# Optimization experiments

Hardware: AMD Instinct MI355X
Metric: run time of the kernel (lower is better)

The kernel has to match this reference:

```python
import jax, jax.numpy as jnp
import numpy as np

TEMPERATURE = 0.07
EPS = 1e-8  # torch CosineSimilarity norm clamp

N, D, NUM_CLASSES = 4096, 768, 128


def setup_inputs() -> dict:
    key = jax.random.key(0)
    k1, k2, k3 = jax.random.split(key, 3)
    img_emb = jax.random.normal(k1, (N, D), dtype=jnp.float32)
    text_emb = jax.random.normal(k2, (N, D), dtype=jnp.float32)
    labels = jax.random.randint(k3, (N,), 0, NUM_CLASSES, dtype=jnp.int64)
    return {"img_emb": img_emb, "text_emb": text_emb, "labels": labels}


def reference(img_emb, text_emb, labels):
    # cosine similarity via normalize + matmul (avoids O(N^2 D) broadcast)
    img_n = img_emb / jnp.maximum(jnp.linalg.norm(img_emb, axis=-1, keepdims=True), EPS)
    txt_n = text_emb / jnp.maximum(jnp.linalg.norm(text_emb, axis=-1, keepdims=True), EPS)
    logits = jnp.einsum('id,jd->ij', img_n, txt_n) / TEMPERATURE  # [N, N]

    pos_mask = (labels[:, None] == labels[None, :]).astype(logits.dtype)  # [N, N]

    img2text = -(pos_mask * jax.nn.log_softmax(logits, axis=1)).sum(1).mean()
    text2img = -(pos_mask * jax.nn.log_softmax(logits, axis=0)).sum(0).mean()
    return (img2text + text2img) / 2
```

## Files before the change

### kernel.cpp

```cpp
#include <hip/hip_runtime.h>
#include <hip/hip_bf16.h>

#define N_ 4096
#define D_ 768
#define NCLS 128
#define BM 128
#define BN 128
#define BK 64
#define NSTEP 12

typedef __bf16 bf16x8 __attribute__((ext_vector_type(8)));
typedef float f32x4 __attribute__((ext_vector_type(4)));
typedef short s16x8 __attribute__((ext_vector_type(8)));

__global__ __launch_bounds__(192) void normalize_kernel(
    const float* __restrict__ img, const float* __restrict__ txt,
    __hip_bfloat16* __restrict__ img_nb, __hip_bfloat16* __restrict__ txt_nb) {
  int b = blockIdx.x;
  const float* s;
  __hip_bfloat16* d;
  if (b < N_) {
    s = img + (size_t)b * D_;
    d = img_nb + (size_t)b * D_;
  } else {
    s = txt + (size_t)(b - N_) * D_;
    d = txt_nb + (size_t)(b - N_) * D_;
  }
  int tid = threadIdx.x;
  float4 v = ((const float4*)s)[tid];
  float ss = v.x * v.x + v.y * v.y + v.z * v.z + v.w * v.w;
#pragma unroll
  for (int m = 32; m; m >>= 1) ss += __shfl_xor(ss, m);
  __shared__ float wsum[3];
  int lane = tid & 63, w = tid >> 6;
  if (lane == 0) wsum[w] = ss;
  __syncthreads();
  float inv = 1.0f / fmaxf(sqrtf(wsum[0] + wsum[1] + wsum[2]), 1e-8f);
  ushort4 o;
  o.x = __bfloat16_as_ushort(__float2bfloat16(v.x * inv));
  o.y = __bfloat16_as_ushort(__float2bfloat16(v.y * inv));
  o.z = __bfloat16_as_ushort(__float2bfloat16(v.z * inv));
  o.w = __bfloat16_as_ushort(__float2bfloat16(v.w * inv));
  ((ushort4*)d)[tid] = o;
}

__global__ __launch_bounds__(256) void gemm_epi_kernel(
    const unsigned short* __restrict__ A, const unsigned short* __restrict__ B,
    const int* __restrict__ labels, float* __restrict__ row_part,
    float* __restrict__ col_part, float* __restrict__ S_part) {
  __shared__ __align__(16) unsigned short As[2][8192];
  __shared__ __align__(16) unsigned short Bs[2][8192];
  __shared__ int labR[BM], labC[BN];
  __shared__ float rbuf[2][BM], cbuf[2][BN];
  __shared__ float sbuf[4];

  const int bx = blockIdx.x, by = blockIdx.y;
  const int tid = threadIdx.x;
  const int lane = tid & 63, wave = tid >> 6;
  const int wr = wave >> 1, wc = wave & 1;
  const int g = lane >> 4, fr = lane & 15;
  const int rowBase = by * BM, colBase = bx * BN;

  if (tid < BM) labR[tid] = labels[rowBase + tid];
  else labC[tid - BM] = labels[colBase + tid - BM];

  const int gq = tid & 7, rbase = tid >> 3;
  const unsigned short* pa = A + (size_t)(rowBase + rbase) * D_ + gq * 8;
  const unsigned short* pb = B + (size_t)(colBase + rbase) * D_ + gq * 8;
  const int wpos = (rbase * 8 + (gq ^ (rbase & 7))) * 8;

  f32x4 acc[4][4] = {};

  s16x8 ra[4], rb[4];
#pragma unroll
  for (int j = 0; j < 4; ++j) {
    ra[j] = *(const s16x8*)(pa + (size_t)(32 * j) * D_);
    rb[j] = *(const s16x8*)(pb + (size_t)(32 * j) * D_);
  }
#pragma unroll
  for (int j = 0; j < 4; ++j) {
    *(s16x8*)&As[0][wpos + j * 2048] = ra[j];
    *(s16x8*)&Bs[0][wpos + j * 2048] = rb[j];
  }
#pragma unroll
  for (int j = 0; j < 4; ++j) {
    ra[j] = *(const s16x8*)(pa + (size_t)(32 * j) * D_ + BK);
    rb[j] = *(const s16x8*)(pb + (size_t)(32 * j) * D_ + BK);
  }
  __syncthreads();

  for (int u = 0; u < NSTEP; ++u) {
    if (u + 1 < NSTEP) {
      unsigned short* aw = As[(u + 1) & 1];
      unsigned short* bw = Bs[(u + 1) & 1];
#pragma unroll
      for (int j = 0; j < 4; ++j) {
        *(s16x8*)&aw[wpos + j * 2048] = ra[j];
        *(s16x8*)&bw[wpos + j * 2048] = rb[j];
      }
    }
    const unsigned short* as_ = As[u & 1];
    const unsigned short* bs_ = Bs[u & 1];
#pragma unroll
    for (int ks = 0; ks < 2; ++ks) {
      const int sw = (ks * 4 + g) ^ (fr & 7);
      bf16x8 af[4], bf[4];
#pragma unroll
      for (int m = 0; m < 4; ++m)
        af[m] = *(const bf16x8*)&as_[((wr * 64 + m * 16 + fr) * 8 + sw) * 8];
#pragma unroll
      for (int n = 0; n < 4; ++n)
        bf[n] = *(const bf16x8*)&bs_[((wc * 64 + n * 16 + fr) * 8 + sw) * 8];
#pragma unroll
      for (int m = 0; m < 4; ++m)
#pragma unroll
        for (int n = 0; n < 4; ++n)
          acc[m][n] = __builtin_amdgcn_mfma_f32_16x16x32_bf16(af[m], bf[n], acc[m][n], 0, 0, 0);
    }
    if (u + 2 < NSTEP) {
      const int k0 = (u + 2) * BK;
#pragma unroll
      for (int j = 0; j < 4; ++j) {
        ra[j] = *(const s16x8*)(pa + (size_t)(32 * j) * D_ + k0);
        rb[j] = *(const s16x8*)(pb + (size_t)(32 * j) * D_ + k0);
      }
    }
    __syncthreads();
  }

  const float scale = 14.285714285714286f;
  float sPart = 0.f;
  float colAcc[4] = {0.f, 0.f, 0.f, 0.f};
#pragma unroll
  for (int m = 0; m < 4; ++m) {
    float ra2[4] = {0.f, 0.f, 0.f, 0.f};
#pragma unroll
    for (int n = 0; n < 4; ++n) {
      int col = wc * 64 + n * 16 + fr;
      int lc = labC[col];
#pragma unroll
      for (int r = 0; r < 4; ++r) {
        float v = acc[m][n][r] * scale;
        float e = __expf(v);
        ra2[r] += e;
        colAcc[n] += e;
        int row = wr * 64 + m * 16 + g * 4 + r;
        if (labR[row] == lc) sPart += v;
      }
    }
#pragma unroll
    for (int r = 0; r < 4; ++r) {
      float x = ra2[r];
      x += __shfl_xor(x, 1);
      x += __shfl_xor(x, 2);
      x += __shfl_xor(x, 4);
      x += __shfl_xor(x, 8);
      if (fr == 0) rbuf[wc][wr * 64 + m * 16 + g * 4 + r] = x;
    }
  }
#pragma unroll
  for (int n = 0; n < 4; ++n) {
    float x = colAcc[n];
    x += __shfl_xor(x, 16);
    x += __shfl_xor(x, 32);
    if (g == 0) cbuf[wr][wc * 64 + n * 16 + fr] = x;
  }
  float s = sPart;
#pragma unroll
  for (int m = 32; m; m >>= 1) s += __shfl_xor(s, m);
  if (lane == 0) sbuf[wave] = s;
  __syncthreads();
  if (tid < BM)
    row_part[(size_t)bx * N_ + rowBase + tid] = rbuf[0][tid] + rbuf[1][tid];
  else
    col_part[(size_t)by * N_ + colBase + (tid - BM)] = cbuf[0][tid - BM] + cbuf[1][tid - BM];
  if (tid == 0) S_part[by * 32 + bx] = sbuf[0] + sbuf[1] + sbuf[2] + sbuf[3];
}

__global__ __launch_bounds__(256) void reduce_kernel(
    const float* __restrict__ row_part, const float* __restrict__ col_part,
    const float* __restrict__ S_part, const int* __restrict__ labels,
    double* __restrict__ partials) {
  __shared__ int hist[NCLS];
  int tid = threadIdx.x;
  if (tid < NCLS) hist[tid] = 0;
  __syncthreads();
  for (int j = tid; j < N_; j += 256) atomicAdd(&hist[labels[j]], 1);
  __syncthreads();

  int i = blockIdx.x * 256 + tid;
  float rs = 0.f, cs = 0.f;
#pragma unroll
  for (int b = 0; b < 32; ++b) {
    rs += row_part[(size_t)b * N_ + i];
    cs += col_part[(size_t)b * N_ + i];
  }
  int cnt = hist[labels[i]];
  double term = (double)cnt * ((double)logf(rs) + (double)logf(cs));
  double sterm = (i < 1024) ? (double)S_part[i] : 0.0;
#pragma unroll
  for (int m = 32; m; m >>= 1) {
    term += __shfl_xor(term, m);
    sterm += __shfl_xor(sterm, m);
  }
  __shared__ double tbuf[4], sb[4];
  int lane = tid & 63, w = tid >> 6;
  if (lane == 0) { tbuf[w] = term; sb[w] = sterm; }
  __syncthreads();
  if (tid == 0) {
    partials[blockIdx.x] = tbuf[0] + tbuf[1] + tbuf[2] + tbuf[3];
    partials[16 + blockIdx.x] = sb[0] + sb[1] + sb[2] + sb[3];
  }
}

__global__ void final_kernel(const double* __restrict__ partials, float* __restrict__ out) {
  double t = 0.0, s = 0.0;
#pragma unroll
  for (int i = 0; i < 16; ++i) {
    t += partials[i];
    s += partials[16 + i];
  }
  out[0] = (float)((t - 2.0 * s) / (2.0 * (double)N_));
}

extern "C" void kernel_launch(void* const* d_in, const int* in_sizes, int n_in,
                              void* d_out, int out_size, void* d_ws, size_t ws_size,
                              hipStream_t stream) {
  const float* img = (const float*)d_in[0];
  const float* txt = (const float*)d_in[1];
  const int* labels = (const int*)d_in[2];
  float* out = (float*)d_out;
  char* ws = (char*)d_ws;

  __hip_bfloat16* img_nb = (__hip_bfloat16*)(ws);
  __hip_bfloat16* txt_nb = (__hip_bfloat16*)(ws + 6291456);
  float* row_part = (float*)(ws + 12582912);
  float* col_part = (float*)(ws + 13107200);
  float* S_part = (float*)(ws + 13631488);
  double* partials = (double*)(ws + 13635584);

  normalize_kernel<<<2 * N_, 192, 0, stream>>>(img, txt, img_nb, txt_nb);
  gemm_epi_kernel<<<dim3(32, 32), 256, 0, stream>>>(
      (const unsigned short*)img_nb, (const unsigned short*)txt_nb, labels,
      row_part, col_part, S_part);
  reduce_kernel<<<16, 256, 0, stream>>>(row_part, col_part, S_part, labels, partials);
  final_kernel<<<1, 1, 0, stream>>>(partials, out);
}
```

Baseline: 56.08 us.

## Use wave-per-row normalize, reorder GEMM LDS reads, fold final reduce into atomics

The normalize kernel now gives each 64-lane wave a whole row, which removes the shared-memory cross-wave reduction and its barrier. The GEMM loop issues the first k-slice LDS reads before the next-stage shared-memory stores, so MFMA work can overlap with those writes. The final single-thread kernel is replaced by a last-block-done pattern using double atomics plus a memset, removing one launch. The trade-off is an added memset launch and atomic ordering that depends on a threadfence.

Result: slower. 59.32 us (+5.8%).

```diff
diff --git a/kernel.cpp b/kernel.cpp
--- a/kernel.cpp
+++ b/kernel.cpp
@@ -13,35 +13,45 @@
 typedef float f32x4 __attribute__((ext_vector_type(4)));
 typedef short s16x8 __attribute__((ext_vector_type(8)));
 
-__global__ __launch_bounds__(192) void normalize_kernel(
+__global__ __launch_bounds__(256) void normalize_kernel(
     const float* __restrict__ img, const float* __restrict__ txt,
     __hip_bfloat16* __restrict__ img_nb, __hip_bfloat16* __restrict__ txt_nb) {
-  int b = blockIdx.x;
+  int idx = blockIdx.x * 4 + (threadIdx.x >> 6);
+  int lane = threadIdx.x & 63;
   const float* s;
   __hip_bfloat16* d;
-  if (b < N_) {
-    s = img + (size_t)b * D_;
-    d = img_nb + (size_t)b * D_;
+  if (idx < N_) {
+    s = img + (size_t)idx * D_;
+    d = img_nb + (size_t)idx * D_;
   } else {
-    s = txt + (size_t)(b - N_) * D_;
-    d = txt_nb + (size_t)(b - N_) * D_;
-  }
-  int tid = threadIdx.x;
-  float4 v = ((const float4*)s)[tid];
-  float ss = v.x * v.x + v.y * v.y + v.z * v.z + v.w * v.w;
+    s = txt + (size_t)(idx - N_) * D_;
+    d = txt_nb + (size_t)(idx - N_) * D_;
+  }
+  float4 v0 = ((const float4*)s)[lane];
+  float4 v1 = ((const float4*)s)[lane + 64];
+  float4 v2 = ((const float4*)s)[lane + 128];
+  float ss = v0.x * v0.x + v0.y * v0.y + v0.z * v0.z + v0.w * v0.w +
+             v1.x * v1.x + v1.y * v1.y + v1.z * v1.z + v1.w * v1.w +
+             v2.x * v2.x + v2.y * v2.y + v2.z * v2.z + v2.w * v2.w;
 #pragma unroll
   for (int m = 32; m; m >>= 1) ss += __shfl_xor(ss, m);
-  __shared__ float wsum[3];
-  int lane = tid & 63, w = tid >> 6;
-  if (lane == 0) wsum[w] = ss;
-  __syncthreads();
-  float inv = 1.0f / fmaxf(sqrtf(wsum[0] + wsum[1] + wsum[2]), 1e-8f);
-  ushort4 o;
-  o.x = __bfloat16_as_ushort(__float2bfloat16(v.x * inv));
-  o.y = __bfloat16_as_ushort(__float2bfloat16(v.y * inv));
-  o.z = __bfloat16_as_ushort(__float2bfloat16(v.z * inv));
-  o.w = __bfloat16_as_ushort(__float2bfloat16(v.w * inv));
-  ((ushort4*)d)[tid] = o;
+  float inv = 1.0f / fmaxf(sqrtf(ss), 1e-8f);
+  ushort4 o0, o1, o2;
+  o0.x = __bfloat16_as_ushort(__float2bfloat16(v0.x * inv));
+  o0.y = __bfloat16_as_ushort(__float2bfloat16(v0.y * inv));
+  o0.z = __bfloat16_as_ushort(__float2bfloat16(v0.z * inv));
+  o0.w = __bfloat16_as_ushort(__float2bfloat16(v0.w * inv));
+  o1.x = __bfloat16_as_ushort(__float2bfloat16(v1.x * inv));
+  o1.y = __bfloat16_as_ushort(__float2bfloat16(v1.y * inv));
+  o1.z = __bfloat16_as_ushort(__float2bfloat16(v1.z * inv));
+  o1.w = __bfloat16_as_ushort(__float2bfloat16(v1.w * inv));
+  o2.x = __bfloat16_as_ushort(__float2bfloat16(v2.x * inv));
+  o2.y = __bfloat16_as_ushort(__float2bfloat16(v2.y * inv));
+  o2.z = __bfloat16_as_ushort(__float2bfloat16(v2.z * inv));
+  o2.w = __bfloat16_as_ushort(__float2bfloat16(v2.w * inv));
+  ((ushort4*)d)[lane] = o0;
+  ((ushort4*)d)[lane + 64] = o1;
+  ((ushort4*)d)[lane + 128] = o2;
 }
 
 __global__ __launch_bounds__(256) void gemm_epi_kernel(
@@ -90,6 +100,18 @@
   __syncthreads();
 
   for (int u = 0; u < NSTEP; ++u) {
+    const unsigned short* as_ = As[u & 1];
+    const unsigned short* bs_ = Bs[u & 1];
+    bf16x8 af[4], bf[4];
+    {
+      const int sw = g ^ (fr & 7);
+#pragma unroll
+      for (int m = 0; m < 4; ++m)
+        af[m] = *(const bf16x8*)&as_[((wr * 64 + m * 16 + fr) * 8 + sw) * 8];
+#pragma unroll
+      for (int n = 0; n < 4; ++n)
+        bf[n] = *(const bf16x8*)&bs_[((wc * 64 + n * 16 + fr) * 8 + sw) * 8];
+    }
     if (u + 1 < NSTEP) {
       unsigned short* aw = As[(u + 1) & 1];
       unsigned short* bw = Bs[(u + 1) & 1];
@@ -99,24 +121,25 @@
         *(s16x8*)&bw[wpos + j * 2048] = rb[j];
       }
     }
-    const unsigned short* as_ = As[u & 1];
-    const unsigned short* bs_ = Bs[u & 1];
-#pragma unroll
-    for (int ks = 0; ks < 2; ++ks) {
-      const int sw = (ks * 4 + g) ^ (fr & 7);
-      bf16x8 af[4], bf[4];
+#pragma unroll
+    for (int m = 0; m < 4; ++m)
+#pragma unroll
+      for (int n = 0; n < 4; ++n)
+        acc[m][n] = __builtin_amdgcn_mfma_f32_16x16x32_bf16(af[m], bf[n], acc[m][n], 0, 0, 0);
+    {
+      const int sw = (4 + g) ^ (fr & 7);
 #pragma unroll
       for (int m = 0; m < 4; ++m)
         af[m] = *(const bf16x8*)&as_[((wr * 64 + m * 16 + fr) * 8 + sw) * 8];
 #pragma unroll
       for (int n = 0; n < 4; ++n)
         bf[n] = *(const bf16x8*)&bs_[((wc * 64 + n * 16 + fr) * 8 + sw) * 8];
-#pragma unroll
-      for (int m = 0; m < 4; ++m)
-#pragma unroll
-        for (int n = 0; n < 4; ++n)
-          acc[m][n] = __builtin_amdgcn_mfma_f32_16x16x32_bf16(af[m], bf[n], acc[m][n], 0, 0, 0);
-    }
+    }
+#pragma unroll
+    for (int m = 0; m < 4; ++m)
+#pragma unroll
+      for (int n = 0; n < 4; ++n)
+        acc[m][n] = __builtin_amdgcn_mfma_f32_16x16x32_bf16(af[m], bf[n], acc[m][n], 0, 0, 0);
     if (u + 2 < NSTEP) {
       const int k0 = (u + 2) * BK;
 #pragma unroll
@@ -180,7 +203,7 @@
 __global__ __launch_bounds__(256) void reduce_kernel(
     const float* __restrict__ row_part, const float* __restrict__ col_part,
     const float* __restrict__ S_part, const int* __restrict__ labels,
-    double* __restrict__ partials) {
+    double* __restrict__ accs, unsigned* __restrict__ cnt, float* __restrict__ out) {
   __shared__ int hist[NCLS];
   int tid = threadIdx.x;
   if (tid < NCLS) hist[tid] = 0;
@@ -195,8 +218,8 @@
     rs += row_part[(size_t)b * N_ + i];
     cs += col_part[(size_t)b * N_ + i];
   }
-  int cnt = hist[labels[i]];
-  double term = (double)cnt * ((double)logf(rs) + (double)logf(cs));
+  int c = hist[labels[i]];
+  double term = (double)c * ((double)logf(rs) + (double)logf(cs));
   double sterm = (i < 1024) ? (double)S_part[i] : 0.0;
 #pragma unroll
   for (int m = 32; m; m >>= 1) {
@@ -208,19 +231,16 @@
   if (lane == 0) { tbuf[w] = term; sb[w] = sterm; }
   __syncthreads();
   if (tid == 0) {
-    partials[blockIdx.x] = tbuf[0] + tbuf[1] + tbuf[2] + tbuf[3];
-    partials[16 + blockIdx.x] = sb[0] + sb[1] + sb[2] + sb[3];
-  }
-}
-
-__global__ void final_kernel(const double* __restrict__ partials, float* __restrict__ out) {
-  double t = 0.0, s = 0.0;
-#pragma unroll
-  for (int i = 0; i < 16; ++i) {
-    t += partials[i];
-    s += partials[16 + i];
-  }
-  out[0] = (float)((t - 2.0 * s) / (2.0 * (double)N_));
+    atomicAdd(&accs[0], tbuf[0] + tbuf[1] + tbuf[2] + tbuf[3]);
+    atomicAdd(&accs[1], sb[0] + sb[1] + sb[2] + sb[3]);
+    __threadfence();
+    unsigned old = atomicAdd(cnt, 1u);
+    if (old == 15u) {
+      double t = atomicAdd(&accs[0], 0.0);
+      double s2 = atomicAdd(&accs[1], 0.0);
+      out[0] = (float)((t - 2.0 * s2) / (2.0 * (double)N_));
+    }
+  }
 }
 
 extern "C" void kernel_launch(void* const* d_in, const int* in_sizes, int n_in,
@@ -237,12 +257,13 @@
   float* row_part = (float*)(ws + 12582912);
   float* col_part = (float*)(ws + 13107200);
   float* S_part = (float*)(ws + 13631488);
-  double* partials = (double*)(ws + 13635584);
-
-  normalize_kernel<<<2 * N_, 192, 0, stream>>>(img, txt, img_nb, txt_nb);
+  double* accs = (double*)(ws + 13635584);
+  unsigned* cnt = (unsigned*)(ws + 13635600);
+
+  hipMemsetAsync(ws + 13635584, 0, 32, stream);
+  normalize_kernel<<<2 * N_ / 4, 256, 0, stream>>>(img, txt, img_nb, txt_nb);
   gemm_epi_kernel<<<dim3(32, 32), 256, 0, stream>>>(
       (const unsigned short*)img_nb, (const unsigned short*)txt_nb, labels,
       row_part, col_part, S_part);
-  reduce_kernel<<<16, 256, 0, stream>>>(row_part, col_part, S_part, labels, partials);
-  final_kernel<<<1, 1, 0, stream>>>(partials, out);
-}
+  reduce_kernel<<<16, 256, 0, stream>>>(row_part, col_part, S_part, labels, accs, cnt, out);
+}
```

## Fold final kernel into reduce, remap GEMM blocks per XCD, prefetch LDS fragments

Applied to the files above, without the earlier changes.

The final single-thread kernel is removed. Reduce blocks now accumulate into double atomics, and the last block (found with a counter) writes the output; the accumulators are zeroed in the normalize kernel. GEMM block indices are remapped so that tiles sharing B columns land on the same XCD, aiming for better L2 reuse. The main loop loads the first k-half fragments from LDS before the shared-memory store of the next tile, so the LDS reads and writes interleave with the MFMAs. The atomic double accumulation makes the summation order nondeterministic.

After: 53.94 us. -3.8%, faster.

```diff
diff --git a/kernel.cpp b/kernel.cpp
--- a/kernel.cpp
+++ b/kernel.cpp
@@ -15,8 +15,14 @@
 
 __global__ __launch_bounds__(192) void normalize_kernel(
     const float* __restrict__ img, const float* __restrict__ txt,
-    __hip_bfloat16* __restrict__ img_nb, __hip_bfloat16* __restrict__ txt_nb) {
+    __hip_bfloat16* __restrict__ img_nb, __hip_bfloat16* __restrict__ txt_nb,
+    double* __restrict__ accs, unsigned* __restrict__ cnt) {
   int b = blockIdx.x;
+  if (b == 0 && threadIdx.x == 0) {
+    accs[0] = 0.0;
+    accs[1] = 0.0;
+    *cnt = 0u;
+  }
   const float* s;
   __hip_bfloat16* d;
   if (b < N_) {
@@ -54,7 +60,10 @@
   __shared__ float rbuf[2][BM], cbuf[2][BN];
   __shared__ float sbuf[4];
 
-  const int bx = blockIdx.x, by = blockIdx.y;
+  const int lin = blockIdx.y * 32 + blockIdx.x;
+  const int xcd = lin & 7, idx = lin >> 3;
+  const int bx = xcd * 4 + (idx & 3), by = idx >> 2;
+
   const int tid = threadIdx.x;
   const int lane = tid & 63, wave = tid >> 6;
   const int wr = wave >> 1, wc = wave & 1;
@@ -90,6 +99,18 @@
   __syncthreads();
 
   for (int u = 0; u < NSTEP; ++u) {
+    const unsigned short* as_ = As[u & 1];
+    const unsigned short* bs_ = Bs[u & 1];
+    bf16x8 af[4], bf[4];
+    {
+      const int sw = g ^ (fr & 7);
+#pragma unroll
+      for (int m = 0; m < 4; ++m)
+        af[m] = *(const bf16x8*)&as_[((wr * 64 + m * 16 + fr) * 8 + sw) * 8];
+#pragma unroll
+      for (int n = 0; n < 4; ++n)
+        bf[n] = *(const bf16x8*)&bs_[((wc * 64 + n * 16 + fr) * 8 + sw) * 8];
+    }
     if (u + 1 < NSTEP) {
       unsigned short* aw = As[(u + 1) & 1];
       unsigned short* bw = Bs[(u + 1) & 1];
@@ -99,24 +120,25 @@
         *(s16x8*)&bw[wpos + j * 2048] = rb[j];
       }
     }
-    const unsigned short* as_ = As[u & 1];
-    const unsigned short* bs_ = Bs[u & 1];
-#pragma unroll
-    for (int ks = 0; ks < 2; ++ks) {
-      const int sw = (ks * 4 + g) ^ (fr & 7);
-      bf16x8 af[4], bf[4];
+#pragma unroll
+    for (int m = 0; m < 4; ++m)
+#pragma unroll
+      for (int n = 0; n < 4; ++n)
+        acc[m][n] = __builtin_amdgcn_mfma_f32_16x16x32_bf16(af[m], bf[n], acc[m][n], 0, 0, 0);
+    {
+      const int sw = (4 + g) ^ (fr & 7);
 #pragma unroll
       for (int m = 0; m < 4; ++m)
         af[m] = *(const bf16x8*)&as_[((wr * 64 + m * 16 + fr) * 8 + sw) * 8];
 #pragma unroll
       for (int n = 0; n < 4; ++n)
         bf[n] = *(const bf16x8*)&bs_[((wc * 64 + n * 16 + fr) * 8 + sw) * 8];
-#pragma unroll
-      for (int m = 0; m < 4; ++m)
-#pragma unroll
-        for (int n = 0; n < 4; ++n)
-          acc[m][n] = __builtin_amdgcn_mfma_f32_16x16x32_bf16(af[m], bf[n], acc[m][n], 0, 0, 0);
-    }
+    }
+#pragma unroll
+    for (int m = 0; m < 4; ++m)
+#pragma unroll
+      for (int n = 0; n < 4; ++n)
+        acc[m][n] = __builtin_amdgcn_mfma_f32_16x16x32_bf16(af[m], bf[n], acc[m][n], 0, 0, 0);
     if (u + 2 < NSTEP) {
       const int k0 = (u + 2) * BK;
 #pragma unroll
@@ -180,7 +202,7 @@
 __global__ __launch_bounds__(256) void reduce_kernel(
     const float* __restrict__ row_part, const float* __restrict__ col_part,
     const float* __restrict__ S_part, const int* __restrict__ labels,
-    double* __restrict__ partials) {
+    double* __restrict__ accs, unsigned* __restrict__ cnt, float* __restrict__ out) {
   __shared__ int hist[NCLS];
   int tid = threadIdx.x;
   if (tid < NCLS) hist[tid] = 0;
@@ -195,8 +217,8 @@
     rs += row_part[(size_t)b * N_ + i];
     cs += col_part[(size_t)b * N_ + i];
   }
-  int cnt = hist[labels[i]];
-  double term = (double)cnt * ((double)logf(rs) + (double)logf(cs));
+  int c = hist[labels[i]];
+  double term = (double)c * ((double)logf(rs) + (double)logf(cs));
   double sterm = (i < 1024) ? (double)S_part[i] : 0.0;
 #pragma unroll
   for (int m = 32; m; m >>= 1) {
@@ -208,19 +230,16 @@
   if (lane == 0) { tbuf[w] = term; sb[w] = sterm; }
   __syncthreads();
   if (tid == 0) {
-    partials[blockIdx.x] = tbuf[0] + tbuf[1] + tbuf[2] + tbuf[3];
-    partials[16 + blockIdx.x] = sb[0] + sb[1] + sb[2] + sb[3];
-  }
-}
-
-__global__ void final_kernel(const double* __restrict__ partials, float* __restrict__ out) {
-  double t = 0.0, s = 0.0;
-#pragma unroll
-  for (int i = 0; i < 16; ++i) {
-    t += partials[i];
-    s += partials[16 + i];
-  }
-  out[0] = (float)((t - 2.0 * s) / (2.0 * (double)N_));
+    atomicAdd(&accs[0], tbuf[0] + tbuf[1] + tbuf[2] + tbuf[3]);
+    atomicAdd(&accs[1], sb[0] + sb[1] + sb[2] + sb[3]);
+    __threadfence();
+    unsigned old = atomicAdd(cnt, 1u);
+    if (old == 15u) {
+      double t = atomicAdd(&accs[0], 0.0);
+      double s2 = atomicAdd(&accs[1], 0.0);
+      out[0] = (float)((t - 2.0 * s2) / (2.0 * (double)N_));
+    }
+  }
 }
 
 extern "C" void kernel_launch(void* const* d_in, const int* in_sizes, int n_in,
@@ -237,12 +256,12 @@
   float* row_part = (float*)(ws + 12582912);
   float* col_part = (float*)(ws + 13107200);
   float* S_part = (float*)(ws + 13631488);
-  double* partials = (double*)(ws + 13635584);
-
-  normalize_kernel<<<2 * N_, 192, 0, stream>>>(img, txt, img_nb, txt_nb);
+  double* accs = (double*)(ws + 13635584);
+  unsigned* cnt = (unsigned*)(ws + 13635600);
+
+  normalize_kernel<<<2 * N_, 192, 0, stream>>>(img, txt, img_nb, txt_nb, accs, cnt);
   gemm_epi_kernel<<<dim3(32, 32), 256, 0, stream>>>(
       (const unsigned short*)img_nb, (const unsigned short*)txt_nb, labels,
       row_part, col_part, S_part);
-  reduce_kernel<<<16, 256, 0, stream>>>(row_part, col_part, S_part, labels, partials);
-  final_kernel<<<1, 1, 0, stream>>>(partials, out);
-}
+  reduce_kernel<<<16, 256, 0, stream>>>(row_part, col_part, S_part, labels, accs, cnt, out);
+}
```
